# Optimization experiments

Measured on AMD Instinct MI355X. Metric: run time of the kernel, lower is better.

Reference implementation:

```python
import jax, jax.numpy as jnp
import numpy as np

D_MODEL = 2048
N_HEADS = 16
DIM_K = 128
DIM_V = 128
D_MID = 6144
STD = 0.02


def setup_inputs() -> dict:
    key = jax.random.key(0)
    k_x, k_wq, k_wo, k_K, k_V = jax.random.split(key, 5)
    B, T = 2, 2048
    x = jax.random.normal(k_x, (B, T, D_MODEL), dtype=jnp.float32)
    # nn.Linear weights: stored as (out, in); we keep jax convention (in, out)
    Wq = jax.random.normal(k_wq, (D_MODEL, N_HEADS * DIM_K), dtype=jnp.float32) * (1.0 / np.sqrt(D_MODEL))
    Wo = jax.random.normal(k_wo, (N_HEADS * DIM_V, D_MODEL), dtype=jnp.float32) * (1.0 / np.sqrt(N_HEADS * DIM_V))
    K = jax.random.normal(k_K, (N_HEADS, D_MID, DIM_K), dtype=jnp.float32) * STD
    V = jax.random.normal(k_V, (N_HEADS, D_MID, DIM_V), dtype=jnp.float32) * STD
    return {"x": x, "Wq": Wq, "Wo": Wo, "K": K, "V": V}


def reference(x, Wq, Wo, K, V):
    B, T, _ = x.shape
    # Q projection: (b,t,d) @ (d, h*dk) -> (b,t,h,dk)
    Q = (x @ Wq).reshape(B, T, N_HEADS, DIM_K)
    # per-head GEMM 1: (b,t,h,dk) x (h,m,dk) -> (b,t,h,m)
    scores = jnp.einsum('bthk,hmk->bthm', Q, K)
    scores = jax.nn.silu(scores)
    # per-head GEMM 2: (b,t,h,m) x (h,m,dv) -> (b,t,h,dv)
    out = jnp.einsum('bthm,hmv->bthv', scores, V)
    out = out.reshape(B, T, N_HEADS * DIM_V)
    return out @ Wo
```

## Files before the change

### kernel.cpp

```cpp
#include <hip/hip_runtime.h>

typedef unsigned short ushort_t;
typedef __attribute__((ext_vector_type(8))) short bf16x8;
typedef __attribute__((ext_vector_type(4))) float f32x4;
typedef __attribute__((ext_vector_type(2))) unsigned int u32x2;

__device__ __forceinline__ unsigned short f2b(float f) {
  unsigned u = __builtin_bit_cast(unsigned, f);
  u += 0x7fffu + ((u >> 16) & 1u);
  return (unsigned short)(u >> 16);
}

__device__ __forceinline__ float silu_f(float x) {
  float e = __builtin_amdgcn_exp2f(x * -1.44269504f);
  return x * __builtin_amdgcn_rcpf(1.0f + e);
}

__device__ __forceinline__ void gload_lds16(const ushort_t* g, ushort_t* l) {
  auto* gp = (const __attribute__((address_space(1))) ushort_t*)g;
  auto* lp = (__attribute__((address_space(3))) ushort_t*)l;
  __builtin_amdgcn_global_load_lds(gp, lp, 16, 0, 0);
}

__device__ __forceinline__ void storeC(float* C, size_t i, float v) { C[i] = v; }
__device__ __forceinline__ void storeC(ushort_t* C, size_t i, float v) { C[i] = f2b(v); }


__global__ __launch_bounds__(256) void cast_f32_bf16_k(const float4* __restrict__ in,
                                                       ushort4* __restrict__ out, int n4) {
  int i = blockIdx.x * 256 + threadIdx.x;
  if (i < n4) {
    float4 v = in[i];
    ushort4 o;
    o.x = f2b(v.x); o.y = f2b(v.y); o.z = f2b(v.z); o.w = f2b(v.w);
    out[i] = o;
  }
}

__global__ __launch_bounds__(256) void transpose_cast_k(const float* __restrict__ in,
                                                        ushort_t* __restrict__ out,
                                                        int rows, int cols) {
  __shared__ float tile[64][65];
  size_t boff = (size_t)blockIdx.z * rows * cols;
  const float* inb = in + boff;
  ushort_t* outb = out + boff;
  int r0 = blockIdx.y * 64, c0 = blockIdx.x * 64;
  int lr = threadIdx.x >> 6, lc = threadIdx.x & 63;
#pragma unroll
  for (int i = 0; i < 16; i++) {
    int r = i * 4 + lr;
    tile[r][lc] = inb[(size_t)(r0 + r) * cols + (c0 + lc)];
  }
  __syncthreads();
#pragma unroll
  for (int i = 0; i < 16; i++) {
    int oc = i * 4 + lr;
    outb[(size_t)(c0 + oc) * rows + (r0 + lc)] = f2b(tile[lc][oc]);
  }
}


template <typename OutT>
__global__ __launch_bounds__(256) void gemm_bt_k(const ushort_t* __restrict__ A,
                                                 const ushort_t* __restrict__ BT,
                                                 OutT* __restrict__ C, int M, int N, int K) {
  __shared__ alignas(16) ushort_t lA[128 * 32];
  __shared__ alignas(16) ushort_t lB[128 * 32];
  int tid = threadIdx.x, lane = tid & 63, wave = tid >> 6;
  int wm = wave >> 1, wn = wave & 1;
  int m0 = blockIdx.y * 128, n0 = blockIdx.x * 128;
  int lr = lane & 15, lk = lane >> 4;
  f32x4 acc[4][4] = {};
  for (int k0 = 0; k0 < K; k0 += 32) {
    __syncthreads();
#pragma unroll
    for (int t = 0; t < 2; t++) {
      int cb = wave * 128 + t * 64;
      int c = cb + lane;
      int r = c >> 2;
      int kc = (c & 3) ^ ((r >> 1) & 3);
      gload_lds16(A + (size_t)(m0 + r) * K + k0 + kc * 8, lA + (size_t)cb * 8);
      gload_lds16(BT + (size_t)(n0 + r) * K + k0 + kc * 8, lB + (size_t)cb * 8);
    }
    __syncthreads();
    bf16x8 aF[4], bF[4];
#pragma unroll
    for (int i = 0; i < 4; i++) {
      int r = wm * 64 + i * 16 + lr;
      int kc = lk ^ ((r >> 1) & 3);
      aF[i] = *(const bf16x8*)(lA + r * 32 + kc * 8);
    }
#pragma unroll
    for (int j = 0; j < 4; j++) {
      int r = wn * 64 + j * 16 + lr;
      int kc = lk ^ ((r >> 1) & 3);
      bF[j] = *(const bf16x8*)(lB + r * 32 + kc * 8);
    }
#pragma unroll
    for (int i = 0; i < 4; i++)
#pragma unroll
      for (int j = 0; j < 4; j++)
        acc[i][j] = __builtin_amdgcn_mfma_f32_16x16x32_bf16(aF[i], bF[j], acc[i][j], 0, 0, 0);
  }
#pragma unroll
  for (int i = 0; i < 4; i++) {
#pragma unroll
    for (int j = 0; j < 4; j++) {
      int row = m0 + wm * 64 + i * 16 + lk * 4;
      int col = n0 + wn * 64 + j * 16 + lr;
#pragma unroll
      for (int r = 0; r < 4; r++) storeC(C, (size_t)(row + r) * N + col, acc[i][j][r]);
    }
  }
}


__global__ __launch_bounds__(256) void fused_mid_k(const ushort_t* __restrict__ Qb,
                                                   const ushort_t* __restrict__ Kb,
                                                   const ushort_t* __restrict__ VTb,
                                                   ushort_t* __restrict__ mid) {
  __shared__ alignas(16) ushort_t lK[2][64 * 128];
  __shared__ alignas(16) ushort_t lV[2][128 * 64];
  __shared__ alignas(16) ushort_t lS[128 * 64];
  int tid = threadIdx.x, lane = tid & 63, wave = tid >> 6;
  int wm = wave >> 1, wn = wave & 1;
  int lr = lane & 15, lk = lane >> 4;
  int id = blockIdx.x;
  int h = (id & 7) * 2 + (id >> 8);
  int t0 = ((id >> 3) & 31) * 128;
  const ushort_t* Qh = Qb + (size_t)t0 * 2048 + h * 128;
  const ushort_t* Kh = Kb + (size_t)h * 6144 * 128;
  const ushort_t* Vh = VTb + (size_t)h * 128 * 6144;

  bf16x8 qF[4][4];
#pragma unroll
  for (int i = 0; i < 4; i++)
#pragma unroll
    for (int ks = 0; ks < 4; ks++)
      qF[i][ks] = *(const bf16x8*)(Qh + (size_t)(wm * 64 + i * 16 + lr) * 2048 + ks * 32 + lk * 8);

#define STAGE(B, M0)                                                              \
  {                                                                               \
    _Pragma("unroll") for (int t = 0; t < 4; t++) {                               \
      int cb = (wave * 4 + t) * 64;                                               \
      int c = cb + lane;                                                          \
      int rk = c >> 4;                                                            \
      int kck = (c & 15) ^ (rk & 15);                                             \
      gload_lds16(Kh + (size_t)((M0) + rk) * 128 + kck * 8, lK[B] + (size_t)cb * 8); \
      int rv = c >> 3;                                                            \
      int kcv = (c & 7) ^ (rv & 7);                                               \
      gload_lds16(Vh + (size_t)rv * 6144 + (M0) + kcv * 8, lV[B] + (size_t)cb * 8);  \
    }                                                                             \
  }

  STAGE(0, 0);

  f32x4 acc[4][4] = {};
  int cur = 0;
  for (int m0 = 0; m0 < 6144; m0 += 64, cur ^= 1) {
    asm volatile("s_waitcnt vmcnt(0)" ::: "memory");
    __builtin_amdgcn_s_barrier();
    asm volatile("" ::: "memory");
    if (m0 + 64 < 6144) STAGE(cur ^ 1, m0 + 64);

    f32x4 s2[2][4] = {};
#pragma unroll
    for (int ks = 0; ks < 4; ks++) {
      bf16x8 kF[2];
#pragma unroll
      for (int j = 0; j < 2; j++) {
        int r = wn * 32 + j * 16 + lr;
        int kc = (ks * 4 + lk) ^ (r & 15);
        kF[j] = *(const bf16x8*)(lK[cur] + r * 128 + kc * 8);
      }
#pragma unroll
      for (int j = 0; j < 2; j++)
#pragma unroll
        for (int i = 0; i < 4; i++)
          s2[j][i] = __builtin_amdgcn_mfma_f32_16x16x32_bf16(kF[j], qF[i][ks], s2[j][i], 0, 0, 0);
    }
#pragma unroll
    for (int j = 0; j < 2; j++) {
#pragma unroll
      for (int i = 0; i < 4; i++) {
        int mb = wn * 32 + j * 16 + lk * 4;
        int t = wm * 64 + i * 16 + lr;
        float v0 = silu_f(s2[j][i][0]), v1 = silu_f(s2[j][i][1]);
        float v2 = silu_f(s2[j][i][2]), v3 = silu_f(s2[j][i][3]);
        unsigned d0, d1;
        asm("v_cvt_pk_bf16_f32 %0, %1, %2" : "=v"(d0) : "v"(v0), "v"(v1));
        asm("v_cvt_pk_bf16_f32 %0, %1, %2" : "=v"(d1) : "v"(v2), "v"(v3));
        int mc = (mb >> 3) ^ (t & 7);
        u32x2 val; val.x = d0; val.y = d1;
        *(u32x2*)(lS + t * 64 + mc * 8 + (mb & 7)) = val;
      }
    }
    asm volatile("s_waitcnt lgkmcnt(0)" ::: "memory");
    __builtin_amdgcn_s_barrier();
    asm volatile("" ::: "memory");
#pragma unroll
    for (int ks = 0; ks < 2; ks++) {
      bf16x8 sF[4], vF[4];
#pragma unroll
      for (int i = 0; i < 4; i++) {
        int r = wm * 64 + i * 16 + lr;
        int kc = (ks * 4 + lk) ^ (r & 7);
        sF[i] = *(const bf16x8*)(lS + r * 64 + kc * 8);
      }
#pragma unroll
      for (int j = 0; j < 4; j++) {
        int r = wn * 64 + j * 16 + lr;
        int kc = (ks * 4 + lk) ^ (r & 7);
        vF[j] = *(const bf16x8*)(lV[cur] + r * 64 + kc * 8);
      }
#pragma unroll
      for (int i = 0; i < 4; i++)
#pragma unroll
        for (int j = 0; j < 4; j++)
          acc[i][j] = __builtin_amdgcn_mfma_f32_16x16x32_bf16(sF[i], vF[j], acc[i][j], 0, 0, 0);
    }
  }
#undef STAGE
#pragma unroll
  for (int i = 0; i < 4; i++) {
#pragma unroll
    for (int j = 0; j < 4; j++) {
      int row = t0 + wm * 64 + i * 16 + lk * 4;
      int col = h * 128 + wn * 64 + j * 16 + lr;
#pragma unroll
      for (int r = 0; r < 4; r++) mid[(size_t)(row + r) * 2048 + col] = f2b(acc[i][j][r]);
    }
  }
}


extern "C" void kernel_launch(void* const* d_in, const int* in_sizes, int n_in,
                              void* d_out, int out_size, void* d_ws, size_t ws_size,
                              hipStream_t stream) {
  const float* x  = (const float*)d_in[0];
  const float* Wq = (const float*)d_in[1];
  const float* Wo = (const float*)d_in[2];
  const float* K  = (const float*)d_in[3];
  const float* V  = (const float*)d_in[4];
  float* out = (float*)d_out;

  ushort_t* xb   = (ushort_t*)d_ws;
  ushort_t* WqT  = xb + 8388608;
  ushort_t* WoT  = WqT + 4194304;
  ushort_t* Kb   = WoT + 4194304;
  ushort_t* VTb  = Kb + 12582912;
  ushort_t* Qb   = VTb + 12582912;
  ushort_t* midb = xb;

  cast_f32_bf16_k<<<8192, 256, 0, stream>>>((const float4*)x, (ushort4*)xb, 2097152);
  cast_f32_bf16_k<<<12288, 256, 0, stream>>>((const float4*)K, (ushort4*)Kb, 3145728);
  transpose_cast_k<<<dim3(32, 32, 1), 256, 0, stream>>>(Wq, WqT, 2048, 2048);
  transpose_cast_k<<<dim3(32, 32, 1), 256, 0, stream>>>(Wo, WoT, 2048, 2048);
  transpose_cast_k<<<dim3(2, 96, 16), 256, 0, stream>>>(V, VTb, 6144, 128);

  gemm_bt_k<ushort_t><<<dim3(16, 32), 256, 0, stream>>>(xb, WqT, Qb, 4096, 2048, 2048);
  fused_mid_k<<<512, 256, 0, stream>>>(Qb, Kb, VTb, midb);
  gemm_bt_k<float><<<dim3(16, 32), 256, 0, stream>>>(midb, WoT, out, 4096, 2048, 2048);
}
```

Before: 418.4 us.

## Keep silu scores in registers in fused kernel; double-buffer GEMM LDS loads

The fused mid kernel now gives each wave its own 32 rows of t across all 64 m values. A permuted K row order lets the GEMM1 output register layout be packed straight into GEMM2 A-operand fragments, which removes the LDS score buffer, its writes and the second barrier per iteration. The generic bf16 GEMM gains double-buffered LDS staging so the next tile's global loads overlap the current tile's MFMAs. In exchange, each wave reads all V tiles from LDS rather than half of them, and register pressure changes.

```diff
diff --git a/kernel.cpp b/kernel.cpp
--- a/kernel.cpp
+++ b/kernel.cpp
@@ -3,7 +3,7 @@
 typedef unsigned short ushort_t;
 typedef __attribute__((ext_vector_type(8))) short bf16x8;
 typedef __attribute__((ext_vector_type(4))) float f32x4;
-typedef __attribute__((ext_vector_type(2))) unsigned int u32x2;
+typedef __attribute__((ext_vector_type(4))) unsigned int u32x4;
 
 __device__ __forceinline__ unsigned short f2b(float f) {
   unsigned u = __builtin_bit_cast(unsigned, f);
@@ -64,37 +64,45 @@
 __global__ __launch_bounds__(256) void gemm_bt_k(const ushort_t* __restrict__ A,
                                                  const ushort_t* __restrict__ BT,
                                                  OutT* __restrict__ C, int M, int N, int K) {
-  __shared__ alignas(16) ushort_t lA[128 * 32];
-  __shared__ alignas(16) ushort_t lB[128 * 32];
+  __shared__ alignas(16) ushort_t lA[2][128 * 32];
+  __shared__ alignas(16) ushort_t lB[2][128 * 32];
   int tid = threadIdx.x, lane = tid & 63, wave = tid >> 6;
   int wm = wave >> 1, wn = wave & 1;
   int m0 = blockIdx.y * 128, n0 = blockIdx.x * 128;
   int lr = lane & 15, lk = lane >> 4;
   f32x4 acc[4][4] = {};
-  for (int k0 = 0; k0 < K; k0 += 32) {
-    __syncthreads();
-#pragma unroll
-    for (int t = 0; t < 2; t++) {
-      int cb = wave * 128 + t * 64;
-      int c = cb + lane;
-      int r = c >> 2;
-      int kc = (c & 3) ^ ((r >> 1) & 3);
-      gload_lds16(A + (size_t)(m0 + r) * K + k0 + kc * 8, lA + (size_t)cb * 8);
-      gload_lds16(BT + (size_t)(n0 + r) * K + k0 + kc * 8, lB + (size_t)cb * 8);
-    }
-    __syncthreads();
+
+#define STG(B, K0)                                                                   \
+  {                                                                                  \
+    _Pragma("unroll") for (int t = 0; t < 2; t++) {                                  \
+      int cb = wave * 128 + t * 64;                                                  \
+      int c = cb + lane;                                                             \
+      int r = c >> 2;                                                                \
+      int kc = (c & 3) ^ ((r >> 1) & 3);                                             \
+      gload_lds16(A + (size_t)(m0 + r) * K + (K0) + kc * 8, lA[B] + (size_t)cb * 8); \
+      gload_lds16(BT + (size_t)(n0 + r) * K + (K0) + kc * 8, lB[B] + (size_t)cb * 8);\
+    }                                                                                \
+  }
+
+  STG(0, 0);
+  int cur = 0;
+  for (int k0 = 0; k0 < K; k0 += 32, cur ^= 1) {
+    asm volatile("s_waitcnt vmcnt(0)" ::: "memory");
+    __builtin_amdgcn_s_barrier();
+    asm volatile("" ::: "memory");
+    if (k0 + 32 < K) STG(cur ^ 1, k0 + 32);
     bf16x8 aF[4], bF[4];
 #pragma unroll
     for (int i = 0; i < 4; i++) {
       int r = wm * 64 + i * 16 + lr;
       int kc = lk ^ ((r >> 1) & 3);
-      aF[i] = *(const bf16x8*)(lA + r * 32 + kc * 8);
+      aF[i] = *(const bf16x8*)(lA[cur] + r * 32 + kc * 8);
     }
 #pragma unroll
     for (int j = 0; j < 4; j++) {
       int r = wn * 64 + j * 16 + lr;
       int kc = lk ^ ((r >> 1) & 3);
-      bF[j] = *(const bf16x8*)(lB + r * 32 + kc * 8);
+      bF[j] = *(const bf16x8*)(lB[cur] + r * 32 + kc * 8);
     }
 #pragma unroll
     for (int i = 0; i < 4; i++)
@@ -102,6 +110,7 @@
       for (int j = 0; j < 4; j++)
         acc[i][j] = __builtin_amdgcn_mfma_f32_16x16x32_bf16(aF[i], bF[j], acc[i][j], 0, 0, 0);
   }
+#undef STG
 #pragma unroll
   for (int i = 0; i < 4; i++) {
 #pragma unroll
@@ -121,9 +130,7 @@
                                                    ushort_t* __restrict__ mid) {
   __shared__ alignas(16) ushort_t lK[2][64 * 128];
   __shared__ alignas(16) ushort_t lV[2][128 * 64];
-  __shared__ alignas(16) ushort_t lS[128 * 64];
   int tid = threadIdx.x, lane = tid & 63, wave = tid >> 6;
-  int wm = wave >> 1, wn = wave & 1;
   int lr = lane & 15, lk = lane >> 4;
   int id = blockIdx.x;
   int h = (id & 7) * 2 + (id >> 8);
@@ -132,30 +139,30 @@
   const ushort_t* Kh = Kb + (size_t)h * 6144 * 128;
   const ushort_t* Vh = VTb + (size_t)h * 128 * 6144;
 
-  bf16x8 qF[4][4];
-#pragma unroll
-  for (int i = 0; i < 4; i++)
+  bf16x8 qF[2][4];
+#pragma unroll
+  for (int tj = 0; tj < 2; tj++)
 #pragma unroll
     for (int ks = 0; ks < 4; ks++)
-      qF[i][ks] = *(const bf16x8*)(Qh + (size_t)(wm * 64 + i * 16 + lr) * 2048 + ks * 32 + lk * 8);
+      qF[tj][ks] = *(const bf16x8*)(Qh + (size_t)(wave * 32 + tj * 16 + lr) * 2048 + ks * 32 + lk * 8);
 
 #define STAGE(B, M0)                                                              \
   {                                                                               \
     _Pragma("unroll") for (int t = 0; t < 4; t++) {                               \
-      int cb = (wave * 4 + t) * 64;                                               \
-      int c = cb + lane;                                                          \
-      int rk = c >> 4;                                                            \
-      int kck = (c & 15) ^ (rk & 15);                                             \
-      gload_lds16(Kh + (size_t)((M0) + rk) * 128 + kck * 8, lK[B] + (size_t)cb * 8); \
-      int rv = c >> 3;                                                            \
-      int kcv = (c & 7) ^ (rv & 7);                                               \
-      gload_lds16(Vh + (size_t)rv * 6144 + (M0) + kcv * 8, lV[B] + (size_t)cb * 8);  \
+      int c = (wave * 4 + t) * 64 + lane;                                         \
+      int ik = c >> 4;                                                            \
+      int pik = (ik & 0x20) | ((ik & 0x0C) << 1) | ((ik & 0x10) >> 2) | (ik & 3); \
+      int sk = (c & 15) ^ (ik & 15);                                              \
+      gload_lds16(Kh + (size_t)((M0) + pik) * 128 + sk * 8, lK[B] + (size_t)c * 8); \
+      int iv = c >> 3;                                                            \
+      int sv = (c & 7) ^ (iv & 7);                                                \
+      gload_lds16(Vh + (size_t)iv * 6144 + (M0) + sv * 8, lV[B] + (size_t)c * 8); \
     }                                                                             \
   }
 
   STAGE(0, 0);
 
-  f32x4 acc[4][4] = {};
+  f32x4 acc[2][8] = {};
   int cur = 0;
   for (int m0 = 0; m0 < 6144; m0 += 64, cur ^= 1) {
     asm volatile("s_waitcnt vmcnt(0)" ::: "memory");
@@ -163,72 +170,60 @@
     asm volatile("" ::: "memory");
     if (m0 + 64 < 6144) STAGE(cur ^ 1, m0 + 64);
 
-    f32x4 s2[2][4] = {};
+    f32x4 s2[4][2] = {};
 #pragma unroll
     for (int ks = 0; ks < 4; ks++) {
-      bf16x8 kF[2];
-#pragma unroll
-      for (int j = 0; j < 2; j++) {
-        int r = wn * 32 + j * 16 + lr;
-        int kc = (ks * 4 + lk) ^ (r & 15);
-        kF[j] = *(const bf16x8*)(lK[cur] + r * 128 + kc * 8);
+      bf16x8 kF[4];
+#pragma unroll
+      for (int mj = 0; mj < 4; mj++)
+        kF[mj] = *(const bf16x8*)(lK[cur] + (mj * 16 + lr) * 128 + (((ks * 4 + lk) ^ lr) * 8));
+#pragma unroll
+      for (int mj = 0; mj < 4; mj++)
+#pragma unroll
+        for (int tj = 0; tj < 2; tj++)
+          s2[mj][tj] = __builtin_amdgcn_mfma_f32_16x16x32_bf16(kF[mj], qF[tj][ks], s2[mj][tj], 0, 0, 0);
+    }
+    unsigned P[4][2][2];
+#pragma unroll
+    for (int mj = 0; mj < 4; mj++) {
+#pragma unroll
+      for (int tj = 0; tj < 2; tj++) {
+        float v0 = silu_f(s2[mj][tj][0]), v1 = silu_f(s2[mj][tj][1]);
+        float v2 = silu_f(s2[mj][tj][2]), v3 = silu_f(s2[mj][tj][3]);
+        asm("v_cvt_pk_bf16_f32 %0, %1, %2" : "=v"(P[mj][tj][0]) : "v"(v0), "v"(v1));
+        asm("v_cvt_pk_bf16_f32 %0, %1, %2" : "=v"(P[mj][tj][1]) : "v"(v2), "v"(v3));
       }
-#pragma unroll
-      for (int j = 0; j < 2; j++)
-#pragma unroll
-        for (int i = 0; i < 4; i++)
-          s2[j][i] = __builtin_amdgcn_mfma_f32_16x16x32_bf16(kF[j], qF[i][ks], s2[j][i], 0, 0, 0);
-    }
-#pragma unroll
-    for (int j = 0; j < 2; j++) {
-#pragma unroll
-      for (int i = 0; i < 4; i++) {
-        int mb = wn * 32 + j * 16 + lk * 4;
-        int t = wm * 64 + i * 16 + lr;
-        float v0 = silu_f(s2[j][i][0]), v1 = silu_f(s2[j][i][1]);
-        float v2 = silu_f(s2[j][i][2]), v3 = silu_f(s2[j][i][3]);
-        unsigned d0, d1;
-        asm("v_cvt_pk_bf16_f32 %0, %1, %2" : "=v"(d0) : "v"(v0), "v"(v1));
-        asm("v_cvt_pk_bf16_f32 %0, %1, %2" : "=v"(d1) : "v"(v2), "v"(v3));
-        int mc = (mb >> 3) ^ (t & 7);
-        u32x2 val; val.x = d0; val.y = d1;
-        *(u32x2*)(lS + t * 64 + mc * 8 + (mb & 7)) = val;
+    }
+#pragma unroll
+    for (int ksg = 0; ksg < 2; ksg++) {
+      bf16x8 aF[2];
+#pragma unroll
+      for (int tj = 0; tj < 2; tj++) {
+        u32x4 w;
+        w.x = P[2 * ksg][tj][0];
+        w.y = P[2 * ksg][tj][1];
+        w.z = P[2 * ksg + 1][tj][0];
+        w.w = P[2 * ksg + 1][tj][1];
+        aF[tj] = __builtin_bit_cast(bf16x8, w);
       }
-    }
-    asm volatile("s_waitcnt lgkmcnt(0)" ::: "memory");
-    __builtin_amdgcn_s_barrier();
-    asm volatile("" ::: "memory");
-#pragma unroll
-    for (int ks = 0; ks < 2; ks++) {
-      bf16x8 sF[4], vF[4];
-#pragma unroll
-      for (int i = 0; i < 4; i++) {
-        int r = wm * 64 + i * 16 + lr;
-        int kc = (ks * 4 + lk) ^ (r & 7);
-        sF[i] = *(const bf16x8*)(lS + r * 64 + kc * 8);
+#pragma unroll
+      for (int vj = 0; vj < 8; vj++) {
+        bf16x8 vF = *(const bf16x8*)(lV[cur] + (vj * 16 + lr) * 64 + (((ksg * 4 + lk) ^ (lr & 7)) * 8));
+#pragma unroll
+        for (int tj = 0; tj < 2; tj++)
+          acc[tj][vj] = __builtin_amdgcn_mfma_f32_16x16x32_bf16(aF[tj], vF, acc[tj][vj], 0, 0, 0);
       }
-#pragma unroll
-      for (int j = 0; j < 4; j++) {
-        int r = wn * 64 + j * 16 + lr;
-        int kc = (ks * 4 + lk) ^ (r & 7);
-        vF[j] = *(const bf16x8*)(lV[cur] + r * 64 + kc * 8);
-      }
-#pragma unroll
-      for (int i = 0; i < 4; i++)
-#pragma unroll
-        for (int j = 0; j < 4; j++)
-          acc[i][j] = __builtin_amdgcn_mfma_f32_16x16x32_bf16(sF[i], vF[j], acc[i][j], 0, 0, 0);
     }
   }
 #undef STAGE
 #pragma unroll
-  for (int i = 0; i < 4; i++) {
-#pragma unroll
-    for (int j = 0; j < 4; j++) {
-      int row = t0 + wm * 64 + i * 16 + lk * 4;
-      int col = h * 128 + wn * 64 + j * 16 + lr;
-#pragma unroll
-      for (int r = 0; r < 4; r++) mid[(size_t)(row + r) * 2048 + col] = f2b(acc[i][j][r]);
+  for (int tj = 0; tj < 2; tj++) {
+#pragma unroll
+    for (int vj = 0; vj < 8; vj++) {
+      int row = t0 + wave * 32 + tj * 16 + lk * 4;
+      int col = h * 128 + vj * 16 + lr;
+#pragma unroll
+      for (int r = 0; r < 4; r++) mid[(size_t)(row + r) * 2048 + col] = f2b(acc[tj][vj][r]);
     }
   }
 }
```

Result: faster. 379.4 us (-9.3%).
